# Optimization experiments

Hardware: AMD Instinct MI355X
Metric: run time of the kernel (lower is better)

Reference implementation:

```python
import jax, jax.numpy as jnp
import numpy as np

B, S, E, H = 32, 256, 768, 32
D = E // H  # head_dim = 24


def setup_inputs() -> dict:
    key = jax.random.key(0)
    ks = jax.random.split(key, 10)
    w_sc = 1.0 / np.sqrt(E)  # xavier-ish init scale for weights
    return {
        "feats": jax.random.normal(ks[0], (B, S, E), jnp.float32),
        "attn_bias": jax.random.normal(ks[1], (B, H, S, S), jnp.float32),
        "delta_pos": jax.random.normal(ks[2], (B, S, S, 3), jnp.float32),
        "Wq": jax.random.normal(ks[3], (E, E), jnp.float32) * w_sc,
        "bq": jnp.zeros((E,), jnp.float32),
        "Wk": jax.random.normal(ks[4], (E, E), jnp.float32) * w_sc,
        "bk": jnp.zeros((E,), jnp.float32),
        "Wv": jax.random.normal(ks[5], (E, E), jnp.float32) * w_sc,
        "bv": jnp.zeros((E,), jnp.float32),
        "Wfx": jax.random.normal(ks[6], (E,), jnp.float32) * w_sc,
        "Wfy": jax.random.normal(ks[7], (E,), jnp.float32) * w_sc,
        "Wfz": jax.random.normal(ks[8], (E,), jnp.float32) * w_sc,
    }


def reference(feats, attn_bias, delta_pos, Wq, bq, Wk, bk, Wv, bv, Wfx, Wfy, Wfz):
    b, s, e = feats.shape
    h = attn_bias.shape[1]
    d = e // h
    scaling = d ** -0.5
    # q/k/v projections; q scaled by 1/sqrt(head_dim)
    q = ((feats @ Wq + bq) * scaling).reshape(b, s, h, d).transpose(0, 2, 1, 3)  # (b,h,s,d)
    k = (feats @ Wk + bk).reshape(b, s, h, d).transpose(0, 2, 1, 3)              # (b,h,t,d)
    v = (feats @ Wv + bv).reshape(b, s, h, d).transpose(0, 2, 1, 3)              # (b,h,t,d)
    scores = jnp.einsum('bhsd,bhtd->bhst', q, k) + attn_bias
    probs = jax.nn.softmax(scores, axis=-1)  # dropout p in eval -> identity
    # rot_attn_probs = probs[...,None] * delta_pos[:,None] fused into one contraction:
    # (b,h,s,t) * (b,s,t,3) contracted with (b,h,t,c) over t -> (b,s,3,h,c)
    attn = jnp.einsum('bhst,bstx,bhtc->bsxhc', probs, delta_pos, v)
    attn = attn.reshape(b, s, 3, e)  # flatten (h,c) -> e
    out_x = attn[..., 0, :] @ Wfx  # (b,s)
    out_y = attn[..., 1, :] @ Wfy
    out_z = attn[..., 2, :] @ Wfz
    return jnp.stack([out_x, out_y, out_z], axis=-1)  # (b,s,3)
```

## Files before the change

### kernel.cpp

```cpp
#include <hip/hip_runtime.h>
#include <hip/hip_bf16.h>

#define B_ 32
#define S_ 256
#define E_ 768
#define H_ 32
#define D_ 24
#define NTOT 1664

typedef __hip_bfloat16 bf16;
typedef __attribute__((ext_vector_type(8))) short short8;
typedef __attribute__((ext_vector_type(4))) float floatx4;
typedef __attribute__((ext_vector_type(2))) float f32x2;

#define GLOAD_LDS16(g, l)                                          \
  __builtin_amdgcn_global_load_lds(                                \
      (const __attribute__((address_space(1))) void*)(g),          \
      (__attribute__((address_space(3))) void*)(l), 16, 0, 0)

__global__ __launch_bounds__(256) void cast_feats(
    const float* __restrict__ in, bf16* __restrict__ outp, int n4)
{
  int i = blockIdx.x * 256 + threadIdx.x;
  if (i < n4) {
    float4 v = reinterpret_cast<const float4*>(in)[i];
    union { ushort4 u; bf16 b[4]; } pk;
    pk.b[0] = (bf16)v.x; pk.b[1] = (bf16)v.y;
    pk.b[2] = (bf16)v.z; pk.b[3] = (bf16)v.w;
    reinterpret_cast<ushort4*>(outp)[i] = pk.u;
  }
}

__global__ __launch_bounds__(256) void prep_qk(
    const float* __restrict__ Wq, const float* __restrict__ Wk,
    bf16* __restrict__ Wt)
{
  __shared__ float tile[64][65];
  int n0 = blockIdx.x * 64;
  int k0 = blockIdx.y * 64;
  int j = threadIdx.x & 63, i4 = threadIdx.x >> 6;
  const float qscale = 0.20412414523193154f;
  bool isq = (n0 < 768);
  const float* W = isq ? Wq : Wk;
  int nc = isq ? n0 : n0 - 768;
  float sc = isq ? qscale : 1.0f;
  #pragma unroll
  for (int r = 0; r < 16; r++) {
    int i = r * 4 + i4;
    tile[i][j] = W[(size_t)(k0 + i) * E_ + nc + j] * sc;
  }
  __syncthreads();
  #pragma unroll
  for (int r = 0; r < 16; r++) {
    int jj = r * 4 + i4;
    Wt[(size_t)(n0 + jj) * E_ + k0 + j] = (bf16)tile[j][jj];
  }
}

__global__ __launch_bounds__(256) void prep_vw_bias(
    const float* __restrict__ Wv,
    const float* __restrict__ bq, const float* __restrict__ bk,
    const float* __restrict__ bv,
    const float* __restrict__ Wfx, const float* __restrict__ Wfy,
    const float* __restrict__ Wfz,
    bf16* __restrict__ Wt, float* __restrict__ biasf)
{
  const float qscale = 0.20412414523193154f;
  int gid = blockIdx.x * 256 + threadIdx.x;
  if (gid < 128 * E_) {
    int n = 1536 + gid / E_, k = gid % E_;
    float val = 0.f;
    if (n < 1632) {
      int nn = n - 1536, x = nn >> 5, h = nn & 31;
      const float* Wf = (x == 0) ? Wfx : (x == 1 ? Wfy : Wfz);
      #pragma unroll
      for (int c = 0; c < D_; c++)
        val += Wv[(size_t)k * E_ + h * D_ + c] * Wf[h * D_ + c];
    }
    Wt[(size_t)n * E_ + k] = (bf16)val;
  } else {
    int n = gid - 128 * E_;
    if (n < NTOT) {
      float val;
      if (n < 768) {
        val = bq[n] * qscale;
      } else if (n < 1536) {
        val = bk[n - 768];
      } else if (n < 1632) {
        int nn = n - 1536, x = nn >> 5, h = nn & 31;
        const float* Wf = (x == 0) ? Wfx : (x == 1 ? Wfy : Wfz);
        float s = 0.f;
        #pragma unroll
        for (int c = 0; c < D_; c++)
          s += bv[h * D_ + c] * Wf[h * D_ + c];
        val = s;
      } else {
        val = 0.f;
      }
      biasf[n] = val;
    }
  }
}

__global__ __launch_bounds__(256) void gemm_qkv(
    const bf16* __restrict__ A, const bf16* __restrict__ Wt,
    const float* __restrict__ biasf,
    bf16* __restrict__ qout, bf16* __restrict__ kout,
    float* __restrict__ vwout)
{
  __shared__ __align__(16) short As[128 * 32];
  __shared__ __align__(16) short Bs[128 * 32];
  int tid = threadIdx.x;
  int m0 = blockIdx.y * 128, n0 = blockIdx.x * 128;
  int wave = tid >> 6, lane = tid & 63;
  int wm = (wave >> 1) * 64, wn = (wave & 1) * 64;
  int fr = lane & 15, quad = lane >> 4;

  int srow = wave * 32 + (lane >> 2);
  int schunk = (lane & 3) ^ (srow & 3);
  const bf16* Asrc = A + (size_t)(m0 + srow) * E_ + schunk * 8;
  const bf16* Bsrc = Wt + (size_t)(n0 + srow) * E_ + schunk * 8;
  short* AsW = As + wave * 1024;
  short* BsW = Bs + wave * 1024;

  floatx4 acc[4][4];
  const floatx4 zero = {0.f, 0.f, 0.f, 0.f};
  #pragma unroll
  for (int i = 0; i < 4; i++)
    #pragma unroll
    for (int j = 0; j < 4; j++) acc[i][j] = zero;

  int ra[4], rb[4];
  #pragma unroll
  for (int t = 0; t < 4; t++) {
    int rowa = wm + t * 16 + fr;
    int rowb = wn + t * 16 + fr;
    ra[t] = rowa * 32 + (quad ^ (rowa & 3)) * 8;
    rb[t] = rowb * 32 + (quad ^ (rowb & 3)) * 8;
  }

  for (int k0 = 0; k0 < E_; k0 += 32) {
    if (k0) __syncthreads();
    GLOAD_LDS16(Asrc + k0, AsW);
    GLOAD_LDS16(Asrc + (size_t)16 * E_ + k0, AsW + 512);
    GLOAD_LDS16(Bsrc + k0, BsW);
    GLOAD_LDS16(Bsrc + (size_t)16 * E_ + k0, BsW + 512);
    __syncthreads();
    short8 af[4], bfr[4];
    #pragma unroll
    for (int t = 0; t < 4; t++)
      af[t] = *reinterpret_cast<const short8*>(&As[ra[t]]);
    #pragma unroll
    for (int t = 0; t < 4; t++)
      bfr[t] = *reinterpret_cast<const short8*>(&Bs[rb[t]]);
    #pragma unroll
    for (int ti = 0; ti < 4; ti++)
      #pragma unroll
      for (int tj = 0; tj < 4; tj++)
        acc[ti][tj] = __builtin_amdgcn_mfma_f32_16x16x32_bf16(
            af[ti], bfr[tj], acc[ti][tj], 0, 0, 0);
  }

  #pragma unroll
  for (int ti = 0; ti < 4; ti++) {
    #pragma unroll
    for (int tj = 0; tj < 4; tj++) {
      int n = n0 + wn + tj * 16 + fr;
      float bias = biasf[n];
      #pragma unroll
      for (int r = 0; r < 4; r++) {
        int m = m0 + wm + ti * 16 + quad * 4 + r;
        int b = m >> 8, s = m & 255;
        float val = acc[ti][tj][r] + bias;
        if (n < 768) {
          qout[(size_t)(b * S_ + s) * E_ + n] = (bf16)val;
        } else if (n < 1536) {
          kout[(size_t)(b * S_ + s) * E_ + (n - 768)] = (bf16)val;
        } else if (n < 1632) {
          int nn = n - 1536, x = nn >> 5, hh = nn & 31;
          vwout[(((size_t)x * B_ + b) * H_ + hh) * S_ + s] = val;
        }
      }
    }
  }
}

__global__ __launch_bounds__(256) void attn_kernel(
    const bf16* __restrict__ qg, const bf16* __restrict__ kg,
    const float* __restrict__ vwg, const float* __restrict__ biasg,
    const float* __restrict__ dpg, float* __restrict__ part)
{
  __shared__ __align__(16) float ql[64 * 26];
  int blk = blockIdx.x;
  int b = blk & 31;
  int u = blk >> 5;
  int h = u & 31;
  int st = (u >> 5) * 64;
  int bh = b * H_ + h;
  int tid = threadIdx.x, wave = tid >> 6, lane = tid & 63;
  int t0 = lane * 4;

  f32x2 kr[4][12];
  #pragma unroll
  for (int j = 0; j < 4; j++) {
    const short8* kp = reinterpret_cast<const short8*>(
        kg + (size_t)(b * S_ + t0 + j) * E_ + h * D_);
    #pragma unroll
    for (int seg = 0; seg < 3; seg++) {
      short8 kk = kp[seg];
      #pragma unroll
      for (int p2 = 0; p2 < 4; p2++) {
        union { short u; bf16 bb; } a, c;
        a.u = kk[2 * p2]; c.u = kk[2 * p2 + 1];
        f32x2 t2; t2.x = (float)a.bb; t2.y = (float)c.bb;
        kr[j][seg * 4 + p2] = t2;
      }
    }
  }
  float vwr[3][4];
  #pragma unroll
  for (int x = 0; x < 3; x++) {
    float4 v4 = *reinterpret_cast<const float4*>(
        vwg + (((size_t)x * B_ + b) * H_ + h) * S_ + t0);
    vwr[x][0] = v4.x; vwr[x][1] = v4.y; vwr[x][2] = v4.z; vwr[x][3] = v4.w;
  }
  {
    int r = tid >> 2, c0 = (tid & 3) * 6;
    const bf16* qrow = qg + (size_t)(b * S_ + st + r) * E_ + h * D_ + c0;
    #pragma unroll
    for (int i = 0; i < 6; i++) ql[r * 26 + c0 + i] = (float)qrow[i];
  }
  __syncthreads();

  const float* biasbh = biasg + (size_t)bh * S_ * S_;
  const float* dpb    = dpg + (size_t)b * S_ * S_ * 3;

  float4 nb, nd0, nd1, nd2;
  {
    int s0 = st + wave;
    nb = *reinterpret_cast<const float4*>(biasbh + (size_t)s0 * S_ + t0);
    const float* dpr = dpb + (size_t)s0 * S_ * 3 + (size_t)t0 * 3;
    nd0 = *reinterpret_cast<const float4*>(dpr);
    nd1 = *reinterpret_cast<const float4*>(dpr + 4);
    nd2 = *reinterpret_cast<const float4*>(dpr + 8);
  }

  for (int si = 0; si < 16; si++) {
    float4 bias4 = nb, e0 = nd0, e1 = nd1, e2 = nd2;
    int nsi = (si + 1 < 16) ? si + 1 : 0;
    int ns = st + nsi * 4 + wave;
    nb = *reinterpret_cast<const float4*>(biasbh + (size_t)ns * S_ + t0);
    const float* dpn = dpb + (size_t)ns * S_ * 3 + (size_t)t0 * 3;
    nd0 = *reinterpret_cast<const float4*>(dpn);
    nd1 = *reinterpret_cast<const float4*>(dpn + 4);
    nd2 = *reinterpret_cast<const float4*>(dpn + 8);

    int sr = si * 4 + wave;
    int s  = st + sr;

    f32x2 sc2[4];
    #pragma unroll
    for (int j = 0; j < 4; j++) { sc2[j].x = 0.f; sc2[j].y = 0.f; }
    #pragma unroll
    for (int i = 0; i < 12; i++) {
      f32x2 qd = *reinterpret_cast<const f32x2*>(&ql[sr * 26 + 2 * i]);
      #pragma unroll
      for (int j = 0; j < 4; j++) sc2[j] += qd * kr[j][i];
    }
    float p[4];
    p[0] = __expf(sc2[0].x + sc2[0].y + bias4.x - 4.0f);
    p[1] = __expf(sc2[1].x + sc2[1].y + bias4.y - 4.0f);
    p[2] = __expf(sc2[2].x + sc2[2].y + bias4.z - 4.0f);
    p[3] = __expf(sc2[3].x + sc2[3].y + bias4.w - 4.0f);
    float l = (p[0] + p[1]) + (p[2] + p[3]);

    float dx[4] = {e0.x, e0.w, e1.z, e2.y};
    float dy[4] = {e0.y, e1.x, e1.w, e2.z};
    float dz[4] = {e0.z, e1.y, e2.x, e2.w};

    float ax = 0.f, ay = 0.f, az = 0.f;
    #pragma unroll
    for (int j = 0; j < 4; j++) {
      ax = fmaf(p[j] * dx[j], vwr[0][j], ax);
      ay = fmaf(p[j] * dy[j], vwr[1][j], ay);
      az = fmaf(p[j] * dz[j], vwr[2][j], az);
    }
    #pragma unroll
    for (int o = 32; o; o >>= 1) {
      ax += __shfl_xor(ax, o);
      ay += __shfl_xor(ay, o);
      az += __shfl_xor(az, o);
      l  += __shfl_xor(l, o);
    }
    if (lane == 0) {
      float inv = 1.0f / l;
      float* op = part + ((size_t)bh * S_ + s) * 3;
      op[0] = ax * inv; op[1] = ay * inv; op[2] = az * inv;
    }
  }
}

__global__ __launch_bounds__(256) void reduce_h(
    const float* __restrict__ part, float* __restrict__ out)
{
  int k = blockIdx.x * 256 + threadIdx.x;
  int b = k / (S_ * 3);
  int r = k - b * (S_ * 3);
  const float* p = part + (size_t)b * H_ * S_ * 3 + r;
  float acc = 0.f;
  #pragma unroll
  for (int h = 0; h < H_; h++) acc += p[(size_t)h * S_ * 3];
  out[k] = acc;
}

extern "C" void kernel_launch(void* const* d_in, const int* in_sizes, int n_in,
                              void* d_out, int out_size, void* d_ws, size_t ws_size,
                              hipStream_t stream)
{
  const float* feats     = (const float*)d_in[0];
  const float* attn_bias = (const float*)d_in[1];
  const float* delta_pos = (const float*)d_in[2];
  const float* Wq        = (const float*)d_in[3];
  const float* bq        = (const float*)d_in[4];
  const float* Wk        = (const float*)d_in[5];
  const float* bk        = (const float*)d_in[6];
  const float* Wv        = (const float*)d_in[7];
  const float* bv        = (const float*)d_in[8];
  const float* Wfx       = (const float*)d_in[9];
  const float* Wfy       = (const float*)d_in[10];
  const float* Wfz       = (const float*)d_in[11];

  char* ws = (char*)d_ws;
  size_t off = 0;
  auto alloc = [&](size_t bytes) -> void* {
    void* p = ws + off;
    off = (off + bytes + 255) & ~(size_t)255;
    return p;
  };
  bf16*  ws_fb   = (bf16*) alloc((size_t)B_ * S_ * E_ * 2);
  bf16*  ws_q    = (bf16*) alloc((size_t)B_ * S_ * E_ * 2);
  bf16*  ws_k    = (bf16*) alloc((size_t)B_ * S_ * E_ * 2);
  float* ws_vw   = (float*)alloc((size_t)3 * B_ * H_ * S_ * 4);
  bf16*  ws_Wt   = (bf16*) alloc((size_t)NTOT * E_ * 2);
  float* ws_bias = (float*)alloc((size_t)NTOT * 4);
  float* ws_part = (float*)alloc((size_t)B_ * H_ * S_ * 3 * 4);

  int n4 = B_ * S_ * E_ / 4;
  cast_feats<<<(n4 + 255) / 256, 256, 0, stream>>>(feats, ws_fb, n4);

  prep_qk<<<dim3(24, 12), 256, 0, stream>>>(Wq, Wk, ws_Wt);

  int prep_n = 128 * E_ + NTOT;
  prep_vw_bias<<<(prep_n + 255) / 256, 256, 0, stream>>>(
      Wv, bq, bk, bv, Wfx, Wfy, Wfz, ws_Wt, ws_bias);

  gemm_qkv<<<dim3(NTOT / 128, B_ * S_ / 128), 256, 0, stream>>>(
      ws_fb, ws_Wt, ws_bias, ws_q, ws_k, ws_vw);

  attn_kernel<<<B_ * H_ * 4, 256, 0, stream>>>(ws_q, ws_k, ws_vw, attn_bias,
                                               delta_pos, ws_part);

  reduce_h<<<(B_ * S_ * 3) / 256, 256, 0, stream>>>(ws_part, (float*)d_out);
}
```

Baseline: 551.5 us.

## Fuse prep kernels into one launch and store Q/K head-major

Merges the feats cast, Q/K weight transpose and V/bias prep kernels into one launch, with block-index ranges selecting each role, to remove two kernel launches. The QKV GEMM epilogue now writes Q and K in a (b,h,s,d) head-major layout. Each attention block therefore reads a contiguous chunk of K and Q instead of rows strided by the embedding size. The cost is scattered, less coalesced bf16 stores in the GEMM epilogue, plus integer divide-by-24 index math there.

```diff
diff --git a/kernel.cpp b/kernel.cpp
--- a/kernel.cpp
+++ b/kernel.cpp
@@ -18,46 +18,13 @@
       (const __attribute__((address_space(1))) void*)(g),          \
       (__attribute__((address_space(3))) void*)(l), 16, 0, 0)
 
-__global__ __launch_bounds__(256) void cast_feats(
-    const float* __restrict__ in, bf16* __restrict__ outp, int n4)
-{
-  int i = blockIdx.x * 256 + threadIdx.x;
-  if (i < n4) {
-    float4 v = reinterpret_cast<const float4*>(in)[i];
-    union { ushort4 u; bf16 b[4]; } pk;
-    pk.b[0] = (bf16)v.x; pk.b[1] = (bf16)v.y;
-    pk.b[2] = (bf16)v.z; pk.b[3] = (bf16)v.w;
-    reinterpret_cast<ushort4*>(outp)[i] = pk.u;
-  }
-}
-
-__global__ __launch_bounds__(256) void prep_qk(
+#define CAST_BLKS 6144
+#define QK_BLKS   288
+#define VW_BLKS   391
+
+__global__ __launch_bounds__(256) void prep_fused(
+    const float* __restrict__ feats, bf16* __restrict__ fb,
     const float* __restrict__ Wq, const float* __restrict__ Wk,
-    bf16* __restrict__ Wt)
-{
-  __shared__ float tile[64][65];
-  int n0 = blockIdx.x * 64;
-  int k0 = blockIdx.y * 64;
-  int j = threadIdx.x & 63, i4 = threadIdx.x >> 6;
-  const float qscale = 0.20412414523193154f;
-  bool isq = (n0 < 768);
-  const float* W = isq ? Wq : Wk;
-  int nc = isq ? n0 : n0 - 768;
-  float sc = isq ? qscale : 1.0f;
-  #pragma unroll
-  for (int r = 0; r < 16; r++) {
-    int i = r * 4 + i4;
-    tile[i][j] = W[(size_t)(k0 + i) * E_ + nc + j] * sc;
-  }
-  __syncthreads();
-  #pragma unroll
-  for (int r = 0; r < 16; r++) {
-    int jj = r * 4 + i4;
-    Wt[(size_t)(n0 + jj) * E_ + k0 + j] = (bf16)tile[j][jj];
-  }
-}
-
-__global__ __launch_bounds__(256) void prep_vw_bias(
     const float* __restrict__ Wv,
     const float* __restrict__ bq, const float* __restrict__ bk,
     const float* __restrict__ bv,
@@ -65,8 +32,42 @@
     const float* __restrict__ Wfz,
     bf16* __restrict__ Wt, float* __restrict__ biasf)
 {
+  __shared__ float tile[64][65];
   const float qscale = 0.20412414523193154f;
-  int gid = blockIdx.x * 256 + threadIdx.x;
+  int bid = blockIdx.x;
+
+  if (bid < CAST_BLKS) {
+    int i = bid * 256 + threadIdx.x;
+    float4 v = reinterpret_cast<const float4*>(feats)[i];
+    union { ushort4 u; bf16 b[4]; } pk;
+    pk.b[0] = (bf16)v.x; pk.b[1] = (bf16)v.y;
+    pk.b[2] = (bf16)v.z; pk.b[3] = (bf16)v.w;
+    reinterpret_cast<ushort4*>(fb)[i] = pk.u;
+    return;
+  }
+  if (bid < CAST_BLKS + QK_BLKS) {
+    int id = bid - CAST_BLKS;
+    int n0 = (id % 24) * 64;
+    int k0 = (id / 24) * 64;
+    int j = threadIdx.x & 63, i4 = threadIdx.x >> 6;
+    bool isq = (n0 < 768);
+    const float* W = isq ? Wq : Wk;
+    int nc = isq ? n0 : n0 - 768;
+    float sc = isq ? qscale : 1.0f;
+    #pragma unroll
+    for (int r = 0; r < 16; r++) {
+      int i = r * 4 + i4;
+      tile[i][j] = W[(size_t)(k0 + i) * E_ + nc + j] * sc;
+    }
+    __syncthreads();
+    #pragma unroll
+    for (int r = 0; r < 16; r++) {
+      int jj = r * 4 + i4;
+      Wt[(size_t)(n0 + jj) * E_ + k0 + j] = (bf16)tile[j][jj];
+    }
+    return;
+  }
+  int gid = (bid - CAST_BLKS - QK_BLKS) * 256 + threadIdx.x;
   if (gid < 128 * E_) {
     int n = 1536 + gid / E_, k = gid % E_;
     float val = 0.f;
@@ -173,9 +174,12 @@
         int b = m >> 8, s = m & 255;
         float val = acc[ti][tj][r] + bias;
         if (n < 768) {
-          qout[(size_t)(b * S_ + s) * E_ + n] = (bf16)val;
+          int h = n / 24, d = n - h * 24;
+          qout[(((size_t)b * H_ + h) * S_ + s) * D_ + d] = (bf16)val;
         } else if (n < 1536) {
-          kout[(size_t)(b * S_ + s) * E_ + (n - 768)] = (bf16)val;
+          int n2 = n - 768;
+          int h = n2 / 24, d = n2 - h * 24;
+          kout[(((size_t)b * H_ + h) * S_ + s) * D_ + d] = (bf16)val;
         } else if (n < 1632) {
           int nn = n - 1536, x = nn >> 5, hh = nn & 31;
           vwout[(((size_t)x * B_ + b) * H_ + hh) * S_ + s] = val;
@@ -201,19 +205,19 @@
   int t0 = lane * 4;
 
   f32x2 kr[4][12];
-  #pragma unroll
-  for (int j = 0; j < 4; j++) {
+  {
     const short8* kp = reinterpret_cast<const short8*>(
-        kg + (size_t)(b * S_ + t0 + j) * E_ + h * D_);
-    #pragma unroll
-    for (int seg = 0; seg < 3; seg++) {
-      short8 kk = kp[seg];
+        kg + ((size_t)bh * S_ + t0) * D_);
+    #pragma unroll
+    for (int v = 0; v < 12; v++) {
+      short8 kk = kp[v];
+      int row = v / 3, seg = v % 3;
       #pragma unroll
       for (int p2 = 0; p2 < 4; p2++) {
         union { short u; bf16 bb; } a, c;
         a.u = kk[2 * p2]; c.u = kk[2 * p2 + 1];
         f32x2 t2; t2.x = (float)a.bb; t2.y = (float)c.bb;
-        kr[j][seg * 4 + p2] = t2;
+        kr[row][seg * 4 + p2] = t2;
       }
     }
   }
@@ -226,7 +230,7 @@
   }
   {
     int r = tid >> 2, c0 = (tid & 3) * 6;
-    const bf16* qrow = qg + (size_t)(b * S_ + st + r) * E_ + h * D_ + c0;
+    const bf16* qrow = qg + ((size_t)bh * S_ + st + r) * D_ + c0;
     #pragma unroll
     for (int i = 0; i < 6; i++) ql[r * 26 + c0 + i] = (float)qrow[i];
   }
@@ -338,21 +342,15 @@
     return p;
   };
   bf16*  ws_fb   = (bf16*) alloc((size_t)B_ * S_ * E_ * 2);
-  bf16*  ws_q    = (bf16*) alloc((size_t)B_ * S_ * E_ * 2);
-  bf16*  ws_k    = (bf16*) alloc((size_t)B_ * S_ * E_ * 2);
+  bf16*  ws_q    = (bf16*) alloc((size_t)B_ * H_ * S_ * D_ * 2);
+  bf16*  ws_k    = (bf16*) alloc((size_t)B_ * H_ * S_ * D_ * 2);
   float* ws_vw   = (float*)alloc((size_t)3 * B_ * H_ * S_ * 4);
   bf16*  ws_Wt   = (bf16*) alloc((size_t)NTOT * E_ * 2);
   float* ws_bias = (float*)alloc((size_t)NTOT * 4);
   float* ws_part = (float*)alloc((size_t)B_ * H_ * S_ * 3 * 4);
 
-  int n4 = B_ * S_ * E_ / 4;
-  cast_feats<<<(n4 + 255) / 256, 256, 0, stream>>>(feats, ws_fb, n4);
-
-  prep_qk<<<dim3(24, 12), 256, 0, stream>>>(Wq, Wk, ws_Wt);
-
-  int prep_n = 128 * E_ + NTOT;
-  prep_vw_bias<<<(prep_n + 255) / 256, 256, 0, stream>>>(
-      Wv, bq, bk, bv, Wfx, Wfy, Wfz, ws_Wt, ws_bias);
+  prep_fused<<<CAST_BLKS + QK_BLKS + VW_BLKS, 256, 0, stream>>>(
+      feats, ws_fb, Wq, Wk, Wv, bq, bk, bv, Wfx, Wfy, Wfz, ws_Wt, ws_bias);
 
   gemm_qkv<<<dim3(NTOT / 128, B_ * S_ / 128), 256, 0, stream>>>(
       ws_fb, ws_Wt, ws_bias, ws_q, ws_k, ws_vw);
```

New measurement: 539.2 us. 2.2% less time.
